# Kernel optimization log

Measured on AMD Instinct MI355X. Metric: run time of the kernel, lower is better.

The kernel has to match this reference:

```python
import jax, jax.numpy as jnp
import numpy as np

DIM = 128
HEADS = 4
WS = 8  # window size
HEAD_DIM = DIM // HEADS
LOG100 = float(np.log(100.0))


def _cpb_constants(ws):
    # log-spaced relative coordinates table, shape [(2ws-1)^2, 2]
    rng = np.arange(-(ws - 1), ws, dtype=np.float32)
    table = np.stack(np.meshgrid(rng, rng, indexing='ij'), axis=-1)  # [2ws-1,2ws-1,2]
    table = table / (ws - 1)
    table = table * 8.0
    table = np.sign(table) * np.log2(np.abs(table) + 1.0) / np.log2(8.0)
    table = table.reshape(-1, 2)
    # relative position index, shape [ws^2, ws^2]
    coords = np.stack(np.meshgrid(np.arange(ws), np.arange(ws), indexing='ij'), axis=0).reshape(2, -1)
    rel = coords[:, :, None] - coords[:, None, :]  # [2, ws^2, ws^2]
    idx = (rel[0] + ws - 1) * (2 * ws - 1) + (rel[1] + ws - 1)
    return jnp.asarray(table), jnp.asarray(idx.astype(np.int32))


def setup_inputs() -> dict:
    key = jax.random.key(0)
    ks = jax.random.split(key, 10)
    B, H, W = 16, 128, 128
    nW = (H // WS) * (W // WS)
    return {
        'x': jax.random.normal(ks[0], (B, H, W, DIM), jnp.float32),
        'mask': jnp.zeros((nW, WS * WS, WS * WS), jnp.float32),
        'qkv_w': jax.random.normal(ks[1], (DIM, 3 * DIM), jnp.float32) * 0.02,
        'q_bias': jax.random.normal(ks[2], (DIM,), jnp.float32) * 0.02,
        'v_bias': jax.random.normal(ks[3], (DIM,), jnp.float32) * 0.02,
        'logit_scale': jnp.full((HEADS,), float(np.log(10.0)), jnp.float32),
        'cpb_w1': jax.random.normal(ks[4], (2, 512), jnp.float32) * 0.02,
        'cpb_b1': jax.random.normal(ks[5], (512,), jnp.float32) * 0.02,
        'cpb_w2': jax.random.normal(ks[6], (512, HEADS), jnp.float32) * 0.02,
        'proj_w': jax.random.normal(ks[7], (DIM, DIM), jnp.float32) * 0.02,
        'proj_b': jax.random.normal(ks[8], (DIM,), jnp.float32) * 0.02,
        'height': 128,
        'width': 128,
    }


def reference(x, mask, qkv_w, q_bias, v_bias, logit_scale, cpb_w1, cpb_b1, cpb_w2, proj_w, proj_b, height, width):
    B = x.shape[0]
    N = WS * WS
    wh, ww = height // WS, width // WS
    nW = wh * ww

    # QKV projection, K has no bias
    qkv_b = jnp.concatenate([q_bias, jnp.zeros_like(q_bias), v_bias])
    qkv = x @ qkv_w + qkv_b  # [B,H,W,3*DIM]

    # fused window partition -> [3, B*nW, heads, N, head_dim]
    qkv = qkv.reshape(B, wh, WS, ww, WS, 3, HEADS, HEAD_DIM)
    qkv = jnp.transpose(qkv, (5, 0, 1, 3, 6, 2, 4, 7)).reshape(3, B * nW, HEADS, N, HEAD_DIM)
    q, k, v = qkv[0], qkv[1], qkv[2]

    # cosine attention with clamped learnable temperature
    q = q / jnp.maximum(jnp.linalg.norm(q, axis=-1, keepdims=True), 1e-12)
    k = k / jnp.maximum(jnp.linalg.norm(k, axis=-1, keepdims=True), 1e-12)
    scale = jnp.exp(jnp.minimum(logit_scale, LOG100))  # [heads]
    attn = jnp.einsum('whqd,whkd->whqk', q, k) * scale[None, :, None, None]

    # continuous relative position bias via small MLP
    table, idx = _cpb_constants(WS)
    bias_tab = jax.nn.relu(table @ cpb_w1 + cpb_b1) @ cpb_w2  # [(2ws-1)^2, heads]
    bias = 16.0 * jax.nn.sigmoid(bias_tab[idx])  # [N, N, heads]
    attn = attn + jnp.transpose(bias, (2, 0, 1))[None]

    # shifted-window mask
    attn = attn.reshape(B, nW, HEADS, N, N) + mask[None, :, None, :, :]
    attn = jax.nn.softmax(attn.reshape(B * nW, HEADS, N, N), axis=-1)

    out = jnp.einsum('whqk,whkd->whqd', attn, v)  # [B*nW, heads, N, head_dim]

    # fused window reverse -> [B, H, W, DIM]
    out = out.reshape(B, wh, ww, HEADS, WS, WS, HEAD_DIM)
    out = jnp.transpose(out, (0, 1, 4, 2, 5, 3, 6)).reshape(B, height, width, DIM)

    return out @ proj_w + proj_b
```

## Files before the change

### kernel.cpp

```cpp
#include <hip/hip_runtime.h>

typedef unsigned short u16;
typedef __bf16 bf16x8 __attribute__((ext_vector_type(8)));
typedef float f32x4 __attribute__((ext_vector_type(4)));
typedef int i32x4 __attribute__((ext_vector_type(4)));
typedef int i32x2 __attribute__((ext_vector_type(2)));
typedef i32x4 i32x4_a __attribute__((may_alias));
typedef i32x2 i32x2_a __attribute__((may_alias));
typedef bf16x8 bf16x8_a __attribute__((may_alias));
typedef f32x4 f32x4_a __attribute__((may_alias));
typedef unsigned long long u64_a __attribute__((may_alias));

__device__ __forceinline__ float bf2f(u16 u) {
  union { unsigned int i; float f; } c;
  c.i = ((unsigned int)u) << 16;
  return c.f;
}
__device__ __forceinline__ u16 f2bf(float f) {
  union { __bf16 h; u16 u; } c;
  c.h = (__bf16)f;
  return c.u;
}
__device__ __forceinline__ float gld(const void* p, int i, int isbf) {
  return isbf ? bf2f(((const u16*)p)[i]) : ((const float*)p)[i];
}
__device__ __forceinline__ int sw(int row, int col, int rs) {
  return row * rs + ((((col >> 3) ^ (row & 7)) << 3) | (col & 7));
}

#define WQKVT_OFF 0
#define PWT_OFF   98304
#define QKVB_OFF  131072
#define BIAS_OFF  132608
#define SCALE_OFF 198144
#define PB_OFF    198160
#define FLAG_OFF  198672

__global__ void swin_detect(const unsigned int* __restrict__ xw,
                            unsigned int* __restrict__ flag) {
  int t = threadIdx.x;
  int cnt = 0;
  for (int i = 0; i < 8; i++) {
    unsigned int w = xw[t * 8 + i];
    unsigned int lo = w & 0xffffu;
    unsigned int e = (lo >> 7) & 0xffu;
    if ((e >= 0x70u && e <= 0x82u) || lo == 0u) cnt++;
  }
  cnt += __shfl_xor(cnt, 1);
  cnt += __shfl_xor(cnt, 2);
  cnt += __shfl_xor(cnt, 4);
  cnt += __shfl_xor(cnt, 8);
  cnt += __shfl_xor(cnt, 16);
  cnt += __shfl_xor(cnt, 32);
  if (t == 0) *flag = (cnt >= 256) ? 1u : 0u;
}

__global__ void swin_setup(const void* __restrict__ qkv_w, const void* __restrict__ q_bias,
                           const void* __restrict__ v_bias, const void* __restrict__ ls,
                           const void* __restrict__ cpb_w1, const void* __restrict__ cpb_b1,
                           const void* __restrict__ cpb_w2, const void* __restrict__ proj_w,
                           const void* __restrict__ proj_b, char* __restrict__ ws) {
  const int b = blockIdx.x, t = threadIdx.x;
  const int isbf = (int)*(const unsigned int*)(ws + FLAG_OFF);
  u16* wqkvF = (u16*)(ws + WQKVT_OFF);
  u16* pwF = (u16*)(ws + PWT_OFF);
  float* qkvb = (float*)(ws + QKVB_OFF);
  float* bias16F = (float*)(ws + BIAS_OFF);
  float* scalef = (float*)(ws + SCALE_OFF);
  float* pbf = (float*)(ws + PB_OFF);

  if (b < 128) {
    int ks = b >> 5, lq = (b >> 3) & 3, j = b & 7;
    for (int c = t; c < 384; c += 256) {
      int sub = c / 96, rr = c % 96;
      int nt = rr >> 4, l16 = rr & 15;
      int addr = (((sub * 6 + nt) * 4 + ks) << 9) + ((lq * 16 + l16) << 3) + j;
      wqkvF[addr] = f2bf(gld(qkv_w, b * 384 + c, isbf));
    }
  } else if (b < 256) {
    int r = b - 128;
    int ks = r >> 5, lq = (r >> 3) & 3, j = r & 7;
    if (t < 128) {
      int sub = t >> 5, rr = t & 31;
      int nt = rr >> 4, l16 = rr & 15;
      int addr = (((sub * 2 + nt) * 4 + ks) << 9) + ((lq * 16 + l16) << 3) + j;
      pwF[addr] = f2bf(gld(proj_w, r * 128 + t, isbf));
    }
  } else if (b == 256) {
    for (int o = t; o < 384; o += 256) {
      float v = 0.f;
      if (o < 128) v = gld(q_bias, o, isbf);
      else if (o >= 256) v = gld(v_bias, o - 256, isbf);
      qkvb[o] = v;
    }
    if (t < 128) pbf[t] = gld(proj_b, t, isbf);
    if (t < 4) scalef[t] = expf(fminf(gld(ls, t, isbf), 4.60517019f));
  } else {
    __shared__ float w1[1024];
    __shared__ float b1[512];
    __shared__ float w2[2048];
    __shared__ float tab[225][4];
    for (int i = t; i < 1024; i += 256) w1[i] = gld(cpb_w1, i, isbf);
    for (int i = t; i < 512; i += 256) b1[i] = gld(cpb_b1, i, isbf);
    for (int i = t; i < 2048; i += 256) w2[i] = gld(cpb_w2, i, isbf);
    __syncthreads();
    if (t < 225) {
      int i = t / 15, j = t % 15;
      float c0, c1;
      {
        float tt = ((float)(i - 7) / 7.0f) * 8.0f;
        float s = (tt > 0.f) ? 1.f : ((tt < 0.f) ? -1.f : 0.f);
        c0 = s * log2f(fabsf(tt) + 1.f) / 3.0f;
      }
      {
        float tt = ((float)(j - 7) / 7.0f) * 8.0f;
        float s = (tt > 0.f) ? 1.f : ((tt < 0.f) ? -1.f : 0.f);
        c1 = s * log2f(fabsf(tt) + 1.f) / 3.0f;
      }
      float acc[4] = {0.f, 0.f, 0.f, 0.f};
      for (int jj = 0; jj < 512; jj++) {
        float h = fmaxf(c0 * w1[jj] + c1 * w1[512 + jj] + b1[jj], 0.f);
        #pragma unroll
        for (int hh = 0; hh < 4; hh++) acc[hh] += h * w2[jj * 4 + hh];
      }
      #pragma unroll
      for (int hh = 0; hh < 4; hh++) tab[t][hh] = acc[hh];
    }
    __syncthreads();
    for (int e = t; e < 4 * 64 * 64; e += 256) {
      int h = e >> 12, mg = (e >> 11) & 1, qt = (e >> 10) & 1;
      int kt = (e >> 8) & 3, lane = (e >> 2) & 63, r = e & 3;
      int q = 32 * mg + 16 * qt + (lane & 15);
      int kk = 16 * kt + 4 * (lane >> 4) + r;
      int dr = (q >> 3) - (kk >> 3) + 7;
      int dc = (q & 7) - (kk & 7) + 7;
      float v = tab[dr * 15 + dc][h];
      bias16F[e] = 16.f / (1.f + expf(-v));
    }
  }
}

#define X_OFF 0
#define Q_OFF 8192
#define K_OFF 16384
#define VT_OFF 24576
#define P_OFF 0
#define AO_OFF 16384

__global__ __launch_bounds__(512, 4) void swin_main(
    const void* __restrict__ x, const void* __restrict__ mask,
    const char* __restrict__ ws, void* __restrict__ out) {
  __shared__ __align__(16) u16 lds[32768];
  const f32x4 fz = {0.f, 0.f, 0.f, 0.f};

  const u16* wqkvF = (const u16*)(ws + WQKVT_OFF);
  const u16* pwF = (const u16*)(ws + PWT_OFF);
  const float* qkvb = (const float*)(ws + QKVB_OFF);
  const float* bias16F = (const float*)(ws + BIAS_OFF);
  const float* scalef = (const float*)(ws + SCALE_OFF);
  const float* pbf = (const float*)(ws + PB_OFF);
  const int isbf = (int)*(const unsigned int*)(ws + FLAG_OFF);

  const int tid = threadIdx.x;
  const int wid = tid >> 6;
  const int lane = tid & 63;
  const int ln16 = lane & 15;
  const int lq = lane >> 4;
  const int q8 = lq << 3;
  const int mg = wid >> 2;
  const int sub = wid & 3;

  const int wi = blockIdx.x;
  const int b = wi >> 8;
  const int rem = wi & 255;
  const int wy = rem >> 4, wx = rem & 15;
  const int xbase = ((b * 128 + wy * 8) * 128 + wx * 8) * 128;

  if (isbf) {
    const u16* xb = (const u16*)x;
    #pragma unroll
    for (int rep = 0; rep < 2; rep++) {
      int ch = tid + rep * 512;
      int token = ch >> 4, dch = ch & 15;
      int r = token >> 3, c = token & 7;
      i32x4 v = *(const i32x4_a*)(xb + xbase + r * 16384 + c * 128 + dch * 8);
      *(i32x4_a*)(lds + X_OFF + sw(token, dch * 8, 128)) = v;
    }
  } else {
    const float* xf = (const float*)x;
    #pragma unroll
    for (int rep = 0; rep < 2; rep++) {
      int ch = tid + rep * 512;
      int token = ch >> 4, dch = ch & 15;
      int r = token >> 3, c = token & 7;
      const float* src = xf + xbase + r * 16384 + c * 128 + dch * 8;
      union { i32x4 v2[2]; float f[8]; } in;
      in.v2[0] = *(const i32x4_a*)(src);
      in.v2[1] = *(const i32x4_a*)(src + 4);
      union { u16 u[8]; i32x4 v; } o;
      #pragma unroll
      for (int d = 0; d < 8; d++) o.u[d] = f2bf(in.f[d]);
      *(i32x4_a*)(lds + X_OFF + sw(token, dch * 8, 128)) = o.v;
    }
  }
  __syncthreads();

  f32x4 acc1[2][6];
  #pragma unroll
  for (int nt = 0; nt < 6; nt++) {
    float bv = qkvb[96 * sub + 16 * nt + ln16];
    f32x4 ci = {bv, bv, bv, bv};
    acc1[0][nt] = ci;
    acc1[1][nt] = ci;
  }

  #pragma unroll
  for (int ks = 0; ks < 4; ks++) {
    bf16x8 a0 = *(const bf16x8_a*)(lds + X_OFF + sw(32 * mg + ln16, 32 * ks + q8, 128));
    bf16x8 a1 = *(const bf16x8_a*)(lds + X_OFF + sw(32 * mg + 16 + ln16, 32 * ks + q8, 128));
    bf16x8 bb[6];
    #pragma unroll
    for (int nt = 0; nt < 6; nt++)
      bb[nt] = *(const bf16x8_a*)(wqkvF + (((sub * 6 + nt) * 4 + ks) << 9) + lane * 8);
    #pragma unroll
    for (int nt = 0; nt < 6; nt++) {
      acc1[0][nt] = __builtin_amdgcn_mfma_f32_16x16x32_bf16(a0, bb[nt], acc1[0][nt], 0, 0, 0);
      acc1[1][nt] = __builtin_amdgcn_mfma_f32_16x16x32_bf16(a1, bb[nt], acc1[1][nt], 0, 0, 0);
    }
  }

  #pragma unroll
  for (int ci = 0; ci < 3; ci++) {
    int n0 = 96 * sub + 32 * ci;
    int type = n0 >> 7;
    int head = (n0 & 127) >> 5;
    int nt0 = 2 * ci, nt1 = nt0 + 1;
    if (type < 2) {
      int base = (type == 0) ? Q_OFF : K_OFF;
      float sh = (type == 0) ? scalef[head] : 1.0f;
      #pragma unroll
      for (int mt = 0; mt < 2; mt++)
        #pragma unroll
        for (int r = 0; r < 4; r++) {
          float x0 = acc1[mt][nt0][r], x1 = acc1[mt][nt1][r];
          float ss = x0 * x0 + x1 * x1;
          ss += __shfl_xor(ss, 1);
          ss += __shfl_xor(ss, 2);
          ss += __shfl_xor(ss, 4);
          ss += __shfl_xor(ss, 8);
          float inv = sh / fmaxf(sqrtf(ss), 1e-12f);
          int row = 32 * mg + 16 * mt + 4 * lq + r;
          lds[base + sw(row, head * 32 + ln16, 128)] = f2bf(x0 * inv);
          lds[base + sw(row, head * 32 + 16 + ln16, 128)] = f2bf(x1 * inv);
        }
    } else {
      #pragma unroll
      for (int mt = 0; mt < 2; mt++) {
        int c0 = 32 * mg + 16 * mt + 4 * lq;
        unsigned int w0 = (unsigned int)f2bf(acc1[mt][nt0][0]) | ((unsigned int)f2bf(acc1[mt][nt0][1]) << 16);
        unsigned int w1 = (unsigned int)f2bf(acc1[mt][nt0][2]) | ((unsigned int)f2bf(acc1[mt][nt0][3]) << 16);
        i32x2 wv = {(int)w0, (int)w1};
        *(i32x2_a*)(lds + VT_OFF + sw(head * 32 + ln16, c0, 64)) = wv;
        unsigned int u0 = (unsigned int)f2bf(acc1[mt][nt1][0]) | ((unsigned int)f2bf(acc1[mt][nt1][1]) << 16);
        unsigned int u1 = (unsigned int)f2bf(acc1[mt][nt1][2]) | ((unsigned int)f2bf(acc1[mt][nt1][3]) << 16);
        i32x2 uv = {(int)u0, (int)u1};
        *(i32x2_a*)(lds + VT_OFF + sw(head * 32 + 16 + ln16, c0, 64)) = uv;
      }
    }
  }
  __syncthreads();

  const int h = sub;
  bf16x8 kf[4], qf[2];
  #pragma unroll
  for (int kt = 0; kt < 4; kt++)
    kf[kt] = *(const bf16x8_a*)(lds + K_OFF + sw(16 * kt + ln16, h * 32 + q8, 128));
  #pragma unroll
  for (int qt = 0; qt < 2; qt++)
    qf[qt] = *(const bf16x8_a*)(lds + Q_OFF + sw(32 * mg + 16 * qt + ln16, h * 32 + q8, 128));

  const u16* mk16 = (const u16*)mask;
  const float* mkf = (const float*)mask;
  f32x4 ST[4][2];
  #pragma unroll
  for (int qt = 0; qt < 2; qt++) {
    int q = 32 * mg + 16 * qt + ln16;
    #pragma unroll
    for (int kt = 0; kt < 4; kt++) {
      f32x4 bv = *(const f32x4_a*)(bias16F + h * 4096 + mg * 2048 + qt * 1024 + kt * 256 + lane * 4);
      int bi = q * 64 + 16 * kt + 4 * lq;
      f32x4 cv;
      if (isbf) {
        u64_a mw = *(const u64_a*)(mk16 + rem * 4096 + bi);
        cv[0] = bv[0] + bf2f((u16)mw);
        cv[1] = bv[1] + bf2f((u16)(mw >> 16));
        cv[2] = bv[2] + bf2f((u16)(mw >> 32));
        cv[3] = bv[3] + bf2f((u16)(mw >> 48));
      } else {
        f32x4 mv = *(const f32x4_a*)(mkf + rem * 4096 + bi);
        cv = bv + mv;
      }
      ST[kt][qt] = cv;
    }
  }
  #pragma unroll
  for (int kt = 0; kt < 4; kt++)
    #pragma unroll
    for (int qt = 0; qt < 2; qt++)
      ST[kt][qt] = __builtin_amdgcn_mfma_f32_16x16x32_bf16(kf[kt], qf[qt], ST[kt][qt], 0, 0, 0);

  #pragma unroll
  for (int qt = 0; qt < 2; qt++) {
    float m = ST[0][qt][0];
    #pragma unroll
    for (int kt = 0; kt < 4; kt++)
      #pragma unroll
      for (int r = 0; r < 4; r++) m = fmaxf(m, ST[kt][qt][r]);
    m = fmaxf(m, __shfl_xor(m, 16));
    m = fmaxf(m, __shfl_xor(m, 32));
    float sum = 0.f;
    #pragma unroll
    for (int kt = 0; kt < 4; kt++)
      #pragma unroll
      for (int r = 0; r < 4; r++) {
        float p = __expf(ST[kt][qt][r] - m);
        ST[kt][qt][r] = p;
        sum += p;
      }
    sum += __shfl_xor(sum, 16);
    sum += __shfl_xor(sum, 32);
    float inv = 1.0f / sum;
    #pragma unroll
    for (int kt = 0; kt < 4; kt++)
      #pragma unroll
      for (int r = 0; r < 4; r++) ST[kt][qt][r] *= inv;
  }
  __syncthreads();

  #pragma unroll
  for (int qt = 0; qt < 2; qt++)
    #pragma unroll
    for (int kt = 0; kt < 4; kt++) {
      int row = 32 * mg + 16 * qt + ln16;
      int col = h * 64 + 16 * kt + 4 * lq;
      unsigned int w0 = (unsigned int)f2bf(ST[kt][qt][0]) | ((unsigned int)f2bf(ST[kt][qt][1]) << 16);
      unsigned int w1 = (unsigned int)f2bf(ST[kt][qt][2]) | ((unsigned int)f2bf(ST[kt][qt][3]) << 16);
      i32x2 wv = {(int)w0, (int)w1};
      *(i32x2_a*)(lds + P_OFF + sw(row, col, 256)) = wv;
    }
  __syncthreads();
  f32x4 O[2][2];
  O[0][0] = fz; O[0][1] = fz; O[1][0] = fz; O[1][1] = fz;
  #pragma unroll
  for (int ks = 0; ks < 2; ks++) {
    bf16x8 pf[2], vf[2];
    #pragma unroll
    for (int mt = 0; mt < 2; mt++)
      pf[mt] = *(const bf16x8_a*)(lds + P_OFF + sw(32 * mg + 16 * mt + ln16, h * 64 + 32 * ks + q8, 256));
    #pragma unroll
    for (int nt = 0; nt < 2; nt++)
      vf[nt] = *(const bf16x8_a*)(lds + VT_OFF + sw(h * 32 + 16 * nt + ln16, 32 * ks + q8, 64));
    #pragma unroll
    for (int mt = 0; mt < 2; mt++)
      #pragma unroll
      for (int nt = 0; nt < 2; nt++)
        O[mt][nt] = __builtin_amdgcn_mfma_f32_16x16x32_bf16(pf[mt], vf[nt], O[mt][nt], 0, 0, 0);
  }
  #pragma unroll
  for (int mt = 0; mt < 2; mt++)
    #pragma unroll
    for (int nt = 0; nt < 2; nt++)
      #pragma unroll
      for (int r = 0; r < 4; r++) {
        int row = 32 * mg + 16 * mt + 4 * lq + r;
        lds[AO_OFF + sw(row, h * 32 + 16 * nt + ln16, 128)] = f2bf(O[mt][nt][r]);
      }
  __syncthreads();

  float pb0 = pbf[32 * sub + ln16];
  float pb1 = pbf[32 * sub + 16 + ln16];
  f32x4 acc3[2][2];
  {
    f32x4 c0 = {pb0, pb0, pb0, pb0};
    f32x4 c1 = {pb1, pb1, pb1, pb1};
    acc3[0][0] = c0; acc3[0][1] = c1; acc3[1][0] = c0; acc3[1][1] = c1;
  }
  #pragma unroll
  for (int ks = 0; ks < 4; ks++) {
    bf16x8 a0 = *(const bf16x8_a*)(lds + AO_OFF + sw(32 * mg + ln16, 32 * ks + q8, 128));
    bf16x8 a1 = *(const bf16x8_a*)(lds + AO_OFF + sw(32 * mg + 16 + ln16, 32 * ks + q8, 128));
    bf16x8 b0 = *(const bf16x8_a*)(pwF + (((sub * 2 + 0) * 4 + ks) << 9) + lane * 8);
    bf16x8 b1 = *(const bf16x8_a*)(pwF + (((sub * 2 + 1) * 4 + ks) << 9) + lane * 8);
    acc3[0][0] = __builtin_amdgcn_mfma_f32_16x16x32_bf16(a0, b0, acc3[0][0], 0, 0, 0);
    acc3[0][1] = __builtin_amdgcn_mfma_f32_16x16x32_bf16(a0, b1, acc3[0][1], 0, 0, 0);
    acc3[1][0] = __builtin_amdgcn_mfma_f32_16x16x32_bf16(a1, b0, acc3[1][0], 0, 0, 0);
    acc3[1][1] = __builtin_amdgcn_mfma_f32_16x16x32_bf16(a1, b1, acc3[1][1], 0, 0, 0);
  }
  if (isbf) {
    u16* ob = (u16*)out;
    #pragma unroll
    for (int mt = 0; mt < 2; mt++)
      #pragma unroll
      for (int r = 0; r < 4; r++) {
        int row = 32 * mg + 16 * mt + 4 * lq + r;
        int o = xbase + (row >> 3) * 16384 + (row & 7) * 128 + 32 * sub;
        ob[o + ln16] = f2bf(acc3[mt][0][r]);
        ob[o + 16 + ln16] = f2bf(acc3[mt][1][r]);
      }
  } else {
    float* of = (float*)out;
    #pragma unroll
    for (int mt = 0; mt < 2; mt++)
      #pragma unroll
      for (int r = 0; r < 4; r++) {
        int row = 32 * mg + 16 * mt + 4 * lq + r;
        int o = xbase + (row >> 3) * 16384 + (row & 7) * 128 + 32 * sub;
        of[o + ln16] = acc3[mt][0][r];
        of[o + 16 + ln16] = acc3[mt][1][r];
      }
  }
}

extern "C" void kernel_launch(void* const* d_in, const int* in_sizes, int n_in,
                              void* d_out, int out_size, void* d_ws, size_t ws_size,
                              hipStream_t stream) {
  const void* x      = d_in[0];
  const void* mask   = d_in[1];
  const void* qkv_w  = d_in[2];
  const void* q_bias = d_in[3];
  const void* v_bias = d_in[4];
  const void* ls     = d_in[5];
  const void* cpb_w1 = d_in[6];
  const void* cpb_b1 = d_in[7];
  const void* cpb_w2 = d_in[8];
  const void* proj_w = d_in[9];
  const void* proj_b = d_in[10];
  const int B = in_sizes[0] / (128 * 128 * 128);

  char* ws = (char*)d_ws;
  swin_detect<<<1, 64, 0, stream>>>((const unsigned int*)x,
                                    (unsigned int*)(ws + FLAG_OFF));
  swin_setup<<<258, 256, 0, stream>>>(qkv_w, q_bias, v_bias, ls, cpb_w1, cpb_b1,
                                      cpb_w2, proj_w, proj_b, ws);
  swin_main<<<B * 256, 512, 0, stream>>>(x, mask, ws, d_out);
}
```

Before: 373.0 us.

## Pre-permute mask into MFMA fragment layout and drop a barrier

Adds a setup kernel that converts the shifted-window mask to fp32 and stores it in the same per-lane fragment order as the bias table, so the main kernel can read bias and mask with contiguous coalesced float4 loads. The main kernel is templated on whether the workspace is large enough for this path. It also moves the mask/bias loads earlier, ahead of the Q/K fragment loads. It removes a __syncthreads between writing P to LDS and reading it back, which relies on each wave reading only its own head's region. The cost is an extra setup launch and 4 MB of workspace traffic.

After: 363.5 us. -2.5%, faster.

```diff
diff --git a/kernel.cpp b/kernel.cpp
--- a/kernel.cpp
+++ b/kernel.cpp
@@ -35,6 +35,8 @@
 #define SCALE_OFF 198144
 #define PB_OFF    198160
 #define FLAG_OFF  198672
+#define MASKF_OFF 200704
+#define MASKF_NEED (200704ull + 4ull * 1024 * 1024)
 
 __global__ void swin_detect(const unsigned int* __restrict__ xw,
                             unsigned int* __restrict__ flag) {
@@ -140,6 +142,21 @@
   }
 }
 
+__global__ void swin_setup_mask(const void* __restrict__ mask, char* __restrict__ ws) {
+  const int w = blockIdx.x, t = threadIdx.x;
+  const int isbf = (int)*(const unsigned int*)(ws + FLAG_OFF);
+  float* maskF = (float*)(ws + MASKF_OFF);
+  #pragma unroll
+  for (int i = 0; i < 16; i++) {
+    int e = t + i * 256;
+    int q = e >> 6, k = e & 63;
+    int mg = q >> 5, qt = (q >> 4) & 1, l16 = q & 15;
+    int kt = k >> 4, lq = (k >> 2) & 3, r = k & 3;
+    int addr = w * 4096 + ((mg * 2 + qt) * 4 + kt) * 256 + ((lq * 16 + l16) << 2) + r;
+    maskF[addr] = gld(mask, w * 4096 + e, isbf);
+  }
+}
+
 #define X_OFF 0
 #define Q_OFF 8192
 #define K_OFF 16384
@@ -147,6 +164,7 @@
 #define P_OFF 0
 #define AO_OFF 16384
 
+template <int MF>
 __global__ __launch_bounds__(512, 4) void swin_main(
     const void* __restrict__ x, const void* __restrict__ mask,
     const char* __restrict__ ws, void* __restrict__ out) {
@@ -271,6 +289,44 @@
   __syncthreads();
 
   const int h = sub;
+  f32x4 ST[4][2];
+  if (MF) {
+    const float* mrow = (const float*)(ws + MASKF_OFF) + rem * 4096;
+    #pragma unroll
+    for (int qt = 0; qt < 2; qt++)
+      #pragma unroll
+      for (int kt = 0; kt < 4; kt++) {
+        int fo = mg * 2048 + qt * 1024 + kt * 256 + lane * 4;
+        f32x4 bv = *(const f32x4_a*)(bias16F + h * 4096 + fo);
+        f32x4 mv = *(const f32x4_a*)(mrow + fo);
+        ST[kt][qt] = bv + mv;
+      }
+  } else {
+    const u16* mk16 = (const u16*)mask;
+    const float* mkf = (const float*)mask;
+    #pragma unroll
+    for (int qt = 0; qt < 2; qt++) {
+      int q = 32 * mg + 16 * qt + ln16;
+      #pragma unroll
+      for (int kt = 0; kt < 4; kt++) {
+        f32x4 bv = *(const f32x4_a*)(bias16F + h * 4096 + mg * 2048 + qt * 1024 + kt * 256 + lane * 4);
+        int bi = q * 64 + 16 * kt + 4 * lq;
+        f32x4 cv;
+        if (isbf) {
+          u64_a mw = *(const u64_a*)(mk16 + rem * 4096 + bi);
+          cv[0] = bv[0] + bf2f((u16)mw);
+          cv[1] = bv[1] + bf2f((u16)(mw >> 16));
+          cv[2] = bv[2] + bf2f((u16)(mw >> 32));
+          cv[3] = bv[3] + bf2f((u16)(mw >> 48));
+        } else {
+          f32x4 mv = *(const f32x4_a*)(mkf + rem * 4096 + bi);
+          cv = bv + mv;
+        }
+        ST[kt][qt] = cv;
+      }
+    }
+  }
+
   bf16x8 kf[4], qf[2];
   #pragma unroll
   for (int kt = 0; kt < 4; kt++)
@@ -279,30 +335,6 @@
   for (int qt = 0; qt < 2; qt++)
     qf[qt] = *(const bf16x8_a*)(lds + Q_OFF + sw(32 * mg + 16 * qt + ln16, h * 32 + q8, 128));
 
-  const u16* mk16 = (const u16*)mask;
-  const float* mkf = (const float*)mask;
-  f32x4 ST[4][2];
-  #pragma unroll
-  for (int qt = 0; qt < 2; qt++) {
-    int q = 32 * mg + 16 * qt + ln16;
-    #pragma unroll
-    for (int kt = 0; kt < 4; kt++) {
-      f32x4 bv = *(const f32x4_a*)(bias16F + h * 4096 + mg * 2048 + qt * 1024 + kt * 256 + lane * 4);
-      int bi = q * 64 + 16 * kt + 4 * lq;
-      f32x4 cv;
-      if (isbf) {
-        u64_a mw = *(const u64_a*)(mk16 + rem * 4096 + bi);
-        cv[0] = bv[0] + bf2f((u16)mw);
-        cv[1] = bv[1] + bf2f((u16)(mw >> 16));
-        cv[2] = bv[2] + bf2f((u16)(mw >> 32));
-        cv[3] = bv[3] + bf2f((u16)(mw >> 48));
-      } else {
-        f32x4 mv = *(const f32x4_a*)(mkf + rem * 4096 + bi);
-        cv = bv + mv;
-      }
-      ST[kt][qt] = cv;
-    }
-  }
   #pragma unroll
   for (int kt = 0; kt < 4; kt++)
     #pragma unroll
@@ -348,7 +380,6 @@
       i32x2 wv = {(int)w0, (int)w1};
       *(i32x2_a*)(lds + P_OFF + sw(row, col, 256)) = wv;
     }
-  __syncthreads();
   f32x4 O[2][2];
   O[0][0] = fz; O[0][1] = fz; O[1][0] = fz; O[1][1] = fz;
   #pragma unroll
@@ -442,5 +473,10 @@
                                     (unsigned int*)(ws + FLAG_OFF));
   swin_setup<<<258, 256, 0, stream>>>(qkv_w, q_bias, v_bias, ls, cpb_w1, cpb_b1,
                                       cpb_w2, proj_w, proj_b, ws);
-  swin_main<<<B * 256, 512, 0, stream>>>(x, mask, ws, d_out);
-}
+  if (ws_size >= MASKF_NEED) {
+    swin_setup_mask<<<256, 256, 0, stream>>>(mask, ws);
+    swin_main<1><<<B * 256, 512, 0, stream>>>(x, mask, ws, d_out);
+  } else {
+    swin_main<0><<<B * 256, 512, 0, stream>>>(x, mask, ws, d_out);
+  }
+}
```
